# Kernel tuning notes

Hardware: AMD Instinct MI355X
Metric: run time of the kernel (lower is better)

The kernel has to match this reference:

```python
import jax, jax.numpy as jnp
import numpy as np

EPS = 1e-7
N_NODES = 100000

# --- Lorentz model (c = 1), working at the origin o = (1, 0, ..., 0) ---

def expmap0(v_spatial):
    """Exp map at origin: tangent spatial part [N, d] -> hyperboloid point [N, d+1]."""
    nrm = jnp.sqrt(jnp.maximum(jnp.sum(v_spatial * v_spatial, axis=-1, keepdims=True), EPS))
    x0 = jnp.cosh(nrm)
    xs = jnp.sinh(nrm) / nrm * v_spatial
    return jnp.concatenate([x0, xs], axis=-1)


def logmap0(x):
    """Log map at origin: point [N, d+1] -> tangent spatial part [N, d]."""
    x0 = jnp.maximum(x[..., :1], 1.0 + EPS)
    xs = x[..., 1:]
    nrm = jnp.sqrt(jnp.maximum(jnp.sum(xs * xs, axis=-1, keepdims=True), EPS))
    return jnp.arccosh(x0) / nrm * xs


def sigmoid_nonlin(x):
    # log map -> sigmoid in tangent space -> exp map (c_in = c_out = 1)
    return expmap0(jax.nn.sigmoid(logmap0(x)))


def hgcn_layer(x, edge_index, W, b):
    """HGCN conv: tangent-space linear + mean aggregation over edges + exp map."""
    t = logmap0(x)                      # [N, d_in]
    h = t @ W + b                       # [N, d_out]
    src, dst = edge_index[0], edge_index[1]
    msg = h[src]                        # [E, d_out] gather
    agg = jax.ops.segment_sum(msg, dst, num_segments=N_NODES)
    deg = jax.ops.segment_sum(jnp.ones((edge_index.shape[1],), h.dtype), dst,
                              num_segments=N_NODES)
    agg = agg / jnp.maximum(deg, 1.0)[:, None]
    return expmap0(agg)


def setup_inputs() -> dict:
    key = jax.random.key(0)
    ks = jax.random.split(key, 10)
    d_in, h1, h2, h_mlp, d_out = 64, 64, 64, 128, 40
    return {
        "features": jax.random.normal(ks[0], (N_NODES, d_in), jnp.float32),
        "edge_index": jax.random.randint(ks[1], (2, 1600000), 0, N_NODES, jnp.int64),
        "W1": jax.random.normal(ks[2], (d_in, h1), jnp.float32) * 0.05,
        "b1": jnp.zeros((h1,), jnp.float32),
        "W2": jax.random.normal(ks[3], (h1, h2), jnp.float32) * 0.05,
        "b2": jnp.zeros((h2,), jnp.float32),
        "W3": jax.random.normal(ks[4], (h2, h_mlp), jnp.float32) * 0.05,
        "b3": jnp.zeros((h_mlp,), jnp.float32),
        "W4": jax.random.normal(ks[5], (h_mlp, d_out), jnp.float32) * 0.05,
        "b4": jnp.zeros((d_out,), jnp.float32),
    }


def reference(features, edge_index, W1, b1, W2, b2, W3, b3, W4, b4):
    # lift Euclidean features to the hyperboloid (pad time coord, exp map)
    x = expmap0(features)                       # [N, d_in+1]
    x = hgcn_layer(x, edge_index, W1, b1)
    x = sigmoid_nonlin(x)
    x = hgcn_layer(x, edge_index, W2, b2)
    x = sigmoid_nonlin(x)
    t = logmap0(x)                              # [N, h2] (spatial part, drops time coord)
    # MLP head (dropout inactive at eval)
    h = jax.nn.relu(t @ W3 + b3)
    return h @ W4 + b4
```

## Files before the change

kernel.cpp:

```cpp
#include <hip/hip_runtime.h>


constexpr int CSHIFT = 9;
constexpr int CNODES = 1 << CSHIFT;
constexpr int EPB    = 4096;
constexpr int EPT    = EPB / 256;
constexpr int CAP    = 16384;

constexpr int W1F_OFF = 0;
constexpr int W2F_OFF = 4096;
constexpr int W3F_OFF = 8192;
constexpr int W4F_OFF = 16384;
constexpr int WIMG_TOT = 22528;

typedef __attribute__((ext_vector_type(8))) short short8;
typedef __attribute__((ext_vector_type(4))) float floatx4;

__device__ __forceinline__ float sigmoidf(float x) {
    return 1.0f / (1.0f + __expf(-x));
}
__device__ __forceinline__ unsigned short f2bf(float f) {
    unsigned int u = __float_as_uint(f);
    u = (u + 0x7FFFu + ((u >> 16) & 1u)) >> 16;
    return (unsigned short)u;
}

__global__ __launch_bounds__(256) void part_prep_k(
    const int* __restrict__ src, const int* __restrict__ dst,
    int* __restrict__ ccur, int* __restrict__ arena, int E, int NBUCK, int gP,
    const float* __restrict__ feat, unsigned short* __restrict__ featbf,
    const float* __restrict__ W1, const float* __restrict__ W2,
    const float* __restrict__ W3, const float* __restrict__ W4,
    unsigned short* __restrict__ img, int n8)
{
    __shared__ int  hist[256];
    __shared__ int  exoff[256];
    __shared__ int  lcur[256];
    __shared__ int  gbase[256];
    __shared__ int  stage[EPB];
    __shared__ unsigned char stageB[EPB];

    const int tid = threadIdx.x;

    if ((int)blockIdx.x >= gP) {
        int i = ((int)blockIdx.x - gP) * 256 + tid;
        if (i < n8) {
            const float4* p = (const float4*)feat + (size_t)i * 2;
            float4 a = p[0], b = p[1];
            uint4 o;
            o.x = (unsigned)f2bf(a.x) | ((unsigned)f2bf(a.y) << 16);
            o.y = (unsigned)f2bf(a.z) | ((unsigned)f2bf(a.w) << 16);
            o.z = (unsigned)f2bf(b.x) | ((unsigned)f2bf(b.y) << 16);
            o.w = (unsigned)f2bf(b.z) | ((unsigned)f2bf(b.w) << 16);
            ((uint4*)featbf)[i] = o;
            return;
        }
        int t = i - n8;
        if (t >= WIMG_TOT) return;
        float v = 0.f;
        int s = t;
        if (s < W2F_OFF) {
            int j = s & 7, m = (s >> 3) & 15, q = (s >> 7) & 3, kk = (s >> 9) & 1, c = s >> 10;
            v = W1[(kk * 32 + q * 8 + j) * 64 + c * 16 + m];
        } else if (s < W3F_OFF) {
            s -= W2F_OFF;
            int j = s & 7, m = (s >> 3) & 15, q = (s >> 7) & 3, kk = (s >> 9) & 1, c = s >> 10;
            v = W2[(kk * 32 + q * 8 + j) * 64 + c * 16 + m];
        } else if (s < W4F_OFF) {
            s -= W3F_OFF;
            int j = s & 7, m = (s >> 3) & 15, q = (s >> 7) & 3, kk = (s >> 9) & 1, c = s >> 10;
            v = W3[(kk * 32 + q * 8 + j) * 128 + c * 16 + m];
        } else {
            s -= W4F_OFF;
            int j = s & 7, m = (s >> 3) & 15, q = (s >> 7) & 3, kk = (s >> 9) & 3, c = s >> 11;
            int n = c * 16 + m;
            if (n < 40) v = W4[(kk * 32 + q * 8 + j) * 40 + n];
        }
        img[t] = f2bf(v);
        return;
    }

    const int e0  = blockIdx.x * EPB;
    const int ec  = min(EPB, E - e0);

    int pk[EPT], bk[EPT];
    hist[tid] = 0;
    __syncthreads();
    #pragma unroll
    for (int j = 0; j < EPT; j++) {
        int idx = tid + j * 256;
        if (idx < ec) {
            int s = src[e0 + idx];
            int d = dst[e0 + idx];
            bk[j] = d >> CSHIFT;
            pk[j] = s | ((d & (CNODES - 1)) << 17);
            atomicAdd(&hist[bk[j]], 1);
        } else bk[j] = -1;
    }
    __syncthreads();
    const int h = hist[tid];
    exoff[tid] = h;
    __syncthreads();
    for (int dd = 1; dd < 256; dd <<= 1) {
        int v = 0;
        if (tid >= dd) v = exoff[tid - dd];
        __syncthreads();
        if (tid >= dd) exoff[tid] += v;
        __syncthreads();
    }
    const int ex = exoff[tid] - h;
    int gb = 0;
    if (tid < NBUCK && h > 0) gb = atomicAdd(ccur + tid, h);
    __syncthreads();
    exoff[tid] = ex;
    lcur[tid]  = ex;
    gbase[tid] = gb;
    __syncthreads();
    #pragma unroll
    for (int j = 0; j < EPT; j++) {
        if (bk[j] >= 0) {
            int l = atomicAdd(&lcur[bk[j]], 1);
            stage[l]  = pk[j];
            stageB[l] = (unsigned char)bk[j];
        }
    }
    __syncthreads();
    for (int i = tid; i < ec; i += 256) {
        int b = stageB[i];
        arena[(size_t)b * CAP + gbase[b] + (i - exoff[b])] = stage[i];
    }
}

__global__ __launch_bounds__(1024) void csr_fine(const int* __restrict__ arena,
                                                 const int* __restrict__ ccur,
                                                 int* __restrict__ off,
                                                 int* __restrict__ ssrc,
                                                 int N, int E, int NBUCK) {
    __shared__ int part[256];
    __shared__ int cnt[CNODES];
    __shared__ int cur[CNODES];
    __shared__ int wpre[8];
    const int b = blockIdx.x;
    const int node0 = b << CSHIFT;
    const int tid = threadIdx.x;
    const int lane = tid & 63, wid = tid >> 6;

    if (tid < 256) part[tid] = (tid < NBUCK) ? ccur[tid] : 0;
    __syncthreads();
    for (int d = 1; d < 256; d <<= 1) {
        int v = 0;
        if (tid < 256 && tid >= d) v = part[tid - d];
        __syncthreads();
        if (tid < 256 && tid >= d) part[tid] += v;
        __syncthreads();
    }
    const int cbeg = (b > 0) ? part[b - 1] : 0;
    const int ec   = min(ccur[b], CAP);
    if (b == 0 && tid == 0) off[N] = E;

    if (tid < CNODES) cnt[tid] = 0;
    __syncthreads();
    const int* pe = arena + (size_t)b * CAP;
    for (int i = tid; i < ec; i += 1024)
        atomicAdd(&cnt[(pe[i] >> 17) & (CNODES - 1)], 1);
    __syncthreads();

    int c = (tid < CNODES) ? cnt[tid] : 0;
    int v = c;
    #pragma unroll
    for (int d = 1; d < 64; d <<= 1) {
        int t = __shfl_up(v, d);
        if (lane >= d) v += t;
    }
    if (tid < CNODES && lane == 63) wpre[wid] = v;
    __syncthreads();
    if (tid == 0) {
        int s = 0;
        #pragma unroll
        for (int k = 0; k < CNODES / 64; k++) { int t = wpre[k]; wpre[k] = s; s += t; }
    }
    __syncthreads();
    if (tid < CNODES) {
        int ex = wpre[wid] + v - c;
        cur[tid] = ex;
        int node = node0 + tid;
        if (node < N) off[node] = cbeg + ex;
    }
    __syncthreads();
    for (int i = tid; i < ec; i += 1024) {
        int p = pe[i];
        int pos = cbeg + atomicAdd(&cur[(p >> 17) & (CNODES - 1)], 1);
        ssrc[pos] = p & 0x1FFFF;
    }
}

#define ACC8(v)                                    \
    acc[0] += __uint_as_float((v).x << 16);        \
    acc[1] += __uint_as_float((v).x & 0xFFFF0000u);\
    acc[2] += __uint_as_float((v).y << 16);        \
    acc[3] += __uint_as_float((v).y & 0xFFFF0000u);\
    acc[4] += __uint_as_float((v).z << 16);        \
    acc[5] += __uint_as_float((v).z & 0xFFFF0000u);\
    acc[6] += __uint_as_float((v).w << 16);        \
    acc[7] += __uint_as_float((v).w & 0xFFFF0000u);

__device__ __forceinline__ void gather_tile_wave(
    const unsigned short* __restrict__ h, const int* __restrict__ off,
    const int* __restrict__ ssrc, unsigned short* Agg, int rowB, int N,
    int w, int lane)
{
    #pragma unroll
    for (int pass = 0; pass < 2; pass++) {
        int rl = w * 16 + pass * 8 + (lane >> 3);
        int g  = rowB + rl;
        int q  = (lane & 7) * 8;
        uint4 p = make_uint4(0u, 0u, 0u, 0u);
        if (g < N) {
            int beg = off[g], end = off[g + 1];
            float acc[8] = {0.f, 0.f, 0.f, 0.f, 0.f, 0.f, 0.f, 0.f};
            int i = beg;
            for (; i + 8 <= end; i += 8) {
                uint4 v0 = *(const uint4*)(h + (size_t)ssrc[i]     * 64 + q);
                uint4 v1 = *(const uint4*)(h + (size_t)ssrc[i + 1] * 64 + q);
                uint4 v2 = *(const uint4*)(h + (size_t)ssrc[i + 2] * 64 + q);
                uint4 v3 = *(const uint4*)(h + (size_t)ssrc[i + 3] * 64 + q);
                uint4 v4 = *(const uint4*)(h + (size_t)ssrc[i + 4] * 64 + q);
                uint4 v5 = *(const uint4*)(h + (size_t)ssrc[i + 5] * 64 + q);
                uint4 v6 = *(const uint4*)(h + (size_t)ssrc[i + 6] * 64 + q);
                uint4 v7 = *(const uint4*)(h + (size_t)ssrc[i + 7] * 64 + q);
                ACC8(v0); ACC8(v1); ACC8(v2); ACC8(v3);
                ACC8(v4); ACC8(v5); ACC8(v6); ACC8(v7);
            }
            for (; i + 2 <= end; i += 2) {
                uint4 v0 = *(const uint4*)(h + (size_t)ssrc[i]     * 64 + q);
                uint4 v1 = *(const uint4*)(h + (size_t)ssrc[i + 1] * 64 + q);
                ACC8(v0); ACC8(v1);
            }
            for (; i < end; i++) {
                uint4 v = *(const uint4*)(h + (size_t)ssrc[i] * 64 + q);
                ACC8(v);
            }
            float inv = __builtin_amdgcn_rcpf((float)max(end - beg, 1));
            p.x = (unsigned)f2bf(acc[0]*inv) | ((unsigned)f2bf(acc[1]*inv) << 16);
            p.y = (unsigned)f2bf(acc[2]*inv) | ((unsigned)f2bf(acc[3]*inv) << 16);
            p.z = (unsigned)f2bf(acc[4]*inv) | ((unsigned)f2bf(acc[5]*inv) << 16);
            p.w = (unsigned)f2bf(acc[6]*inv) | ((unsigned)f2bf(acc[7]*inv) << 16);
        }
        *(uint4*)(Agg + rl * 72 + q) = p;
    }
}

__global__ __launch_bounds__(128) void aggemm1_k(
    const unsigned short* __restrict__ featbf, const int* __restrict__ off,
    const int* __restrict__ ssrc, const unsigned short* __restrict__ img,
    const float* __restrict__ bias, unsigned short* __restrict__ t1, int N)
{
    __shared__ alignas(16) unsigned short Agg[32 * 72];

    const int tid = threadIdx.x;
    const int rowB = blockIdx.x * 32;
    const int w = tid >> 6, lane = tid & 63;
    const int m = lane & 15, quad = lane >> 4;
    const int row0 = rowB + w * 16;

    gather_tile_wave(featbf, off, ssrc, Agg, rowB, N, w, lane);

    const short8* Wf = (const short8*)(img + W1F_OFF);
    floatx4 acc[4];
    #pragma unroll
    for (int c = 0; c < 4; c++) acc[c] = (floatx4){0.f, 0.f, 0.f, 0.f};
    #pragma unroll
    for (int kk = 0; kk < 2; kk++) {
        short8 a = *(const short8*)(Agg + (w * 16 + m) * 72 + kk * 32 + quad * 8);
        #pragma unroll
        for (int c = 0; c < 4; c++) {
            short8 b = Wf[((c * 2 + kk) * 4 + quad) * 16 + m];
            acc[c] = __builtin_amdgcn_mfma_f32_16x16x32_bf16(a, b, acc[c], 0, 0, 0);
        }
    }
    bool dzr[4];
    int rows[4];
    #pragma unroll
    for (int r = 0; r < 4; r++) {
        rows[r] = row0 + quad * 4 + r;
        dzr[r] = (rows[r] < N) ? (off[rows[r] + 1] == off[rows[r]]) : false;
    }
    #pragma unroll
    for (int c = 0; c < 4; c++) {
        int col = c * 16 + m;
        float bv = bias[col];
        #pragma unroll
        for (int r = 0; r < 4; r++) {
            if (rows[r] < N) {
                float v = dzr[r] ? 0.5f : sigmoidf(acc[c][r] + bv);
                t1[(size_t)rows[r] * 64 + col] = f2bf(v);
            }
        }
    }
}

__global__ __launch_bounds__(128) void aggep3_k(
    const unsigned short* __restrict__ t1, const int* __restrict__ off,
    const int* __restrict__ ssrc, const unsigned short* __restrict__ img,
    const float* __restrict__ b2, const float* __restrict__ b3,
    const float* __restrict__ b4, float* __restrict__ out, int N)
{
    __shared__ alignas(16) unsigned short SM[4608];
    unsigned short* T2  = SM;
    unsigned short* Agg = SM + 2304;
    unsigned short* H3h = SM + 2304;

    const int tid = threadIdx.x;
    const int rowB = blockIdx.x * 32;
    const int w = tid >> 6, lane = tid & 63;
    const int m = lane & 15, quad = lane >> 4;
    const int row0 = rowB + w * 16;

    gather_tile_wave(t1, off, ssrc, Agg, rowB, N, w, lane);

    {
        const short8* Wf = (const short8*)(img + W2F_OFF);
        floatx4 acc[4];
        #pragma unroll
        for (int c = 0; c < 4; c++) acc[c] = (floatx4){0.f, 0.f, 0.f, 0.f};
        #pragma unroll
        for (int kk = 0; kk < 2; kk++) {
            short8 a = *(const short8*)(Agg + (w * 16 + m) * 72 + kk * 32 + quad * 8);
            #pragma unroll
            for (int c = 0; c < 4; c++) {
                short8 b = Wf[((c * 2 + kk) * 4 + quad) * 16 + m];
                acc[c] = __builtin_amdgcn_mfma_f32_16x16x32_bf16(a, b, acc[c], 0, 0, 0);
            }
        }
        bool dzr[4];
        #pragma unroll
        for (int r = 0; r < 4; r++) {
            int row = row0 + quad * 4 + r;
            dzr[r] = (row < N) ? (off[row + 1] == off[row]) : false;
        }
        #pragma unroll
        for (int c = 0; c < 4; c++) {
            int col = c * 16 + m;
            float bv = b2[col];
            #pragma unroll
            for (int r = 0; r < 4; r++) {
                int rl = w * 16 + quad * 4 + r;
                float v = dzr[r] ? 0.5f : sigmoidf(acc[c][r] + bv);
                T2[rl * 72 + col] = f2bf(v);
            }
        }
    }

    floatx4 acc2[3];
    #pragma unroll
    for (int c = 0; c < 3; c++) acc2[c] = (floatx4){0.f, 0.f, 0.f, 0.f};
    const short8* Wf3 = (const short8*)(img + W3F_OFF);
    const short8* Wf4 = (const short8*)(img + W4F_OFF);

    #pragma unroll
    for (int half = 0; half < 2; half++) {
        floatx4 acc[4];
        #pragma unroll
        for (int c = 0; c < 4; c++) acc[c] = (floatx4){0.f, 0.f, 0.f, 0.f};
        #pragma unroll
        for (int kk = 0; kk < 2; kk++) {
            short8 a = *(const short8*)(T2 + (w * 16 + m) * 72 + kk * 32 + quad * 8);
            #pragma unroll
            for (int c = 0; c < 4; c++) {
                short8 b = Wf3[(((half * 4 + c) * 2 + kk) * 4 + quad) * 16 + m];
                acc[c] = __builtin_amdgcn_mfma_f32_16x16x32_bf16(a, b, acc[c], 0, 0, 0);
            }
        }
        #pragma unroll
        for (int c = 0; c < 4; c++) {
            int col = c * 16 + m;
            float bv = b3[half * 64 + col];
            #pragma unroll
            for (int r = 0; r < 4; r++) {
                int rl = w * 16 + quad * 4 + r;
                H3h[rl * 72 + col] = f2bf(fmaxf(acc[c][r] + bv, 0.f));
            }
        }
        #pragma unroll
        for (int kk2 = 0; kk2 < 2; kk2++) {
            short8 a = *(const short8*)(H3h + (w * 16 + m) * 72 + kk2 * 32 + quad * 8);
            #pragma unroll
            for (int c = 0; c < 3; c++) {
                short8 b = Wf4[((c * 4 + half * 2 + kk2) * 4 + quad) * 16 + m];
                acc2[c] = __builtin_amdgcn_mfma_f32_16x16x32_bf16(a, b, acc2[c], 0, 0, 0);
            }
        }
    }

    #pragma unroll
    for (int c = 0; c < 3; c++) {
        int col = c * 16 + m;
        if (col < 40) {
            float bv = b4[col];
            #pragma unroll
            for (int r = 0; r < 4; r++) {
                int row = row0 + quad * 4 + r;
                if (row < N) out[(size_t)row * 40 + col] = acc2[c][r] + bv;
            }
        }
    }
}

extern "C" void kernel_launch(void* const* d_in, const int* in_sizes, int n_in,
                              void* d_out, int out_size, void* d_ws, size_t ws_size,
                              hipStream_t stream)
{
    const float* feat = (const float*)d_in[0];
    const int*   eidx = (const int*)d_in[1];
    const float* W1 = (const float*)d_in[2];
    const float* b1 = (const float*)d_in[3];
    const float* W2 = (const float*)d_in[4];
    const float* b2 = (const float*)d_in[5];
    const float* W3 = (const float*)d_in[6];
    const float* b3 = (const float*)d_in[7];
    const float* W4 = (const float*)d_in[8];
    const float* b4 = (const float*)d_in[9];

    const int N = in_sizes[0] / 64;
    const int E = in_sizes[1] / 2;
    const int* src = eidx;
    const int* dst = eidx + E;

    const int NBUCK = (N + CNODES - 1) / CNODES;

    unsigned short* featbf = (unsigned short*)d_ws;
    unsigned short* t1     = featbf + (size_t)N * 64;
    unsigned short* img    = t1     + (size_t)N * 64;
    int*   off   = (int*)(img + WIMG_TOT);
    int*   ccur  = off + (N + 1);
    int*   ssrc  = ccur + NBUCK;
    int*   arena = ssrc + E;
    float* out   = (float*)d_out;

    hipMemsetAsync(ccur, 0, (size_t)NBUCK * sizeof(int), stream);

    const dim3 blk(256);
    const int gP  = (E + EPB - 1) / EPB;
    const int g32 = (N + 31) / 32;
    const int n8  = N * 64 / 8;
    const int gPC = (n8 + WIMG_TOT + 255) / 256;

    part_prep_k<<<gP + gPC, blk, 0, stream>>>(src, dst, ccur, arena, E, NBUCK,
                                              gP, feat, featbf, W1, W2, W3, W4,
                                              img, n8);
    csr_fine<<<NBUCK, dim3(1024), 0, stream>>>(arena, ccur, off, ssrc, N, E, NBUCK);

    aggemm1_k<<<g32, dim3(128), 0, stream>>>(featbf, off, ssrc, img, b1, t1, N);
    aggep3_k<<<g32, dim3(128), 0, stream>>>(t1, off, ssrc, img, b2, b3, b4, out, N);
}
```

Measured before the change: 219.1 us.

## Widen partition kernel, use wave-shuffle scan, deepen gather unroll

Raises the partition/prep kernel to 512 threads per block, so each thread handles fewer edges and the conversion blocks cover more elements. It also replaces the shared-memory Hillis-Steele bucket scan, which synchronised on every step, with a wave-level shuffle scan plus a tiny per-wave prefix. Separately, the neighbour gather loop now loads 16 source indices first and then issues 16 row loads, with a 4-wide remainder loop, to put more memory requests in flight. The costs are higher register pressure in the gather and fewer concurrent partition blocks per CU.

```diff
diff --git a/kernel.cpp b/kernel.cpp
--- a/kernel.cpp
+++ b/kernel.cpp
@@ -4,7 +4,8 @@
 constexpr int CSHIFT = 9;
 constexpr int CNODES = 1 << CSHIFT;
 constexpr int EPB    = 4096;
-constexpr int EPT    = EPB / 256;
+constexpr int PTHR   = 512;
+constexpr int EPT    = EPB / PTHR;
 constexpr int CAP    = 16384;
 
 constexpr int W1F_OFF = 0;
@@ -25,7 +26,7 @@
     return (unsigned short)u;
 }
 
-__global__ __launch_bounds__(256) void part_prep_k(
+__global__ __launch_bounds__(512) void part_prep_k(
     const int* __restrict__ src, const int* __restrict__ dst,
     int* __restrict__ ccur, int* __restrict__ arena, int E, int NBUCK, int gP,
     const float* __restrict__ feat, unsigned short* __restrict__ featbf,
@@ -37,13 +38,14 @@
     __shared__ int  exoff[256];
     __shared__ int  lcur[256];
     __shared__ int  gbase[256];
+    __shared__ int  wsum[4];
     __shared__ int  stage[EPB];
     __shared__ unsigned char stageB[EPB];
 
     const int tid = threadIdx.x;
 
     if ((int)blockIdx.x >= gP) {
-        int i = ((int)blockIdx.x - gP) * 256 + tid;
+        int i = ((int)blockIdx.x - gP) * PTHR + tid;
         if (i < n8) {
             const float4* p = (const float4*)feat + (size_t)i * 2;
             float4 a = p[0], b = p[1];
@@ -82,13 +84,14 @@
 
     const int e0  = blockIdx.x * EPB;
     const int ec  = min(EPB, E - e0);
+    const int lane = tid & 63, wid = tid >> 6;
 
     int pk[EPT], bk[EPT];
-    hist[tid] = 0;
+    if (tid < 256) hist[tid] = 0;
     __syncthreads();
     #pragma unroll
     for (int j = 0; j < EPT; j++) {
-        int idx = tid + j * 256;
+        int idx = tid + j * PTHR;
         if (idx < ec) {
             int s = src[e0 + idx];
             int d = dst[e0 + idx];
@@ -98,23 +101,32 @@
         } else bk[j] = -1;
     }
     __syncthreads();
-    const int h = hist[tid];
-    exoff[tid] = h;
-    __syncthreads();
-    for (int dd = 1; dd < 256; dd <<= 1) {
-        int v = 0;
-        if (tid >= dd) v = exoff[tid - dd];
-        __syncthreads();
-        if (tid >= dd) exoff[tid] += v;
-        __syncthreads();
-    }
-    const int ex = exoff[tid] - h;
-    int gb = 0;
-    if (tid < NBUCK && h > 0) gb = atomicAdd(ccur + tid, h);
-    __syncthreads();
-    exoff[tid] = ex;
-    lcur[tid]  = ex;
-    gbase[tid] = gb;
+    int h = 0, v = 0;
+    if (tid < 256) {
+        h = hist[tid];
+        v = h;
+        #pragma unroll
+        for (int d = 1; d < 64; d <<= 1) {
+            int t = __shfl_up(v, d);
+            if (lane >= d) v += t;
+        }
+        if (lane == 63) wsum[wid] = v;
+    }
+    __syncthreads();
+    if (tid == 0) {
+        int s = 0;
+        #pragma unroll
+        for (int k = 0; k < 4; k++) { int t = wsum[k]; wsum[k] = s; s += t; }
+    }
+    __syncthreads();
+    if (tid < 256) {
+        int ex = wsum[wid] + v - h;
+        int gb = 0;
+        if (tid < NBUCK && h > 0) gb = atomicAdd(ccur + tid, h);
+        exoff[tid] = ex;
+        lcur[tid]  = ex;
+        gbase[tid] = gb;
+    }
     __syncthreads();
     #pragma unroll
     for (int j = 0; j < EPT; j++) {
@@ -125,7 +137,7 @@
         }
     }
     __syncthreads();
-    for (int i = tid; i < ec; i += 256) {
+    for (int i = tid; i < ec; i += PTHR) {
         int b = stageB[i];
         arena[(size_t)b * CAP + gbase[b] + (i - exoff[b])] = stage[i];
     }
@@ -219,22 +231,44 @@
             int beg = off[g], end = off[g + 1];
             float acc[8] = {0.f, 0.f, 0.f, 0.f, 0.f, 0.f, 0.f, 0.f};
             int i = beg;
-            for (; i + 8 <= end; i += 8) {
-                uint4 v0 = *(const uint4*)(h + (size_t)ssrc[i]     * 64 + q);
-                uint4 v1 = *(const uint4*)(h + (size_t)ssrc[i + 1] * 64 + q);
-                uint4 v2 = *(const uint4*)(h + (size_t)ssrc[i + 2] * 64 + q);
-                uint4 v3 = *(const uint4*)(h + (size_t)ssrc[i + 3] * 64 + q);
-                uint4 v4 = *(const uint4*)(h + (size_t)ssrc[i + 4] * 64 + q);
-                uint4 v5 = *(const uint4*)(h + (size_t)ssrc[i + 5] * 64 + q);
-                uint4 v6 = *(const uint4*)(h + (size_t)ssrc[i + 6] * 64 + q);
-                uint4 v7 = *(const uint4*)(h + (size_t)ssrc[i + 7] * 64 + q);
+            for (; i + 16 <= end; i += 16) {
+                int s0 = ssrc[i],      s1 = ssrc[i + 1];
+                int s2 = ssrc[i + 2],  s3 = ssrc[i + 3];
+                int s4 = ssrc[i + 4],  s5 = ssrc[i + 5];
+                int s6 = ssrc[i + 6],  s7 = ssrc[i + 7];
+                int s8 = ssrc[i + 8],  s9 = ssrc[i + 9];
+                int sa = ssrc[i + 10], sb = ssrc[i + 11];
+                int sc = ssrc[i + 12], sd = ssrc[i + 13];
+                int se = ssrc[i + 14], sf = ssrc[i + 15];
+                uint4 v0 = *(const uint4*)(h + (size_t)s0 * 64 + q);
+                uint4 v1 = *(const uint4*)(h + (size_t)s1 * 64 + q);
+                uint4 v2 = *(const uint4*)(h + (size_t)s2 * 64 + q);
+                uint4 v3 = *(const uint4*)(h + (size_t)s3 * 64 + q);
+                uint4 v4 = *(const uint4*)(h + (size_t)s4 * 64 + q);
+                uint4 v5 = *(const uint4*)(h + (size_t)s5 * 64 + q);
+                uint4 v6 = *(const uint4*)(h + (size_t)s6 * 64 + q);
+                uint4 v7 = *(const uint4*)(h + (size_t)s7 * 64 + q);
+                uint4 v8 = *(const uint4*)(h + (size_t)s8 * 64 + q);
+                uint4 v9 = *(const uint4*)(h + (size_t)s9 * 64 + q);
+                uint4 va = *(const uint4*)(h + (size_t)sa * 64 + q);
+                uint4 vb = *(const uint4*)(h + (size_t)sb * 64 + q);
+                uint4 vc = *(const uint4*)(h + (size_t)sc * 64 + q);
+                uint4 vd = *(const uint4*)(h + (size_t)sd * 64 + q);
+                uint4 ve = *(const uint4*)(h + (size_t)se * 64 + q);
+                uint4 vf = *(const uint4*)(h + (size_t)sf * 64 + q);
                 ACC8(v0); ACC8(v1); ACC8(v2); ACC8(v3);
                 ACC8(v4); ACC8(v5); ACC8(v6); ACC8(v7);
-            }
-            for (; i + 2 <= end; i += 2) {
-                uint4 v0 = *(const uint4*)(h + (size_t)ssrc[i]     * 64 + q);
-                uint4 v1 = *(const uint4*)(h + (size_t)ssrc[i + 1] * 64 + q);
-                ACC8(v0); ACC8(v1);
+                ACC8(v8); ACC8(v9); ACC8(va); ACC8(vb);
+                ACC8(vc); ACC8(vd); ACC8(ve); ACC8(vf);
+            }
+            for (; i + 4 <= end; i += 4) {
+                int s0 = ssrc[i],     s1 = ssrc[i + 1];
+                int s2 = ssrc[i + 2], s3 = ssrc[i + 3];
+                uint4 v0 = *(const uint4*)(h + (size_t)s0 * 64 + q);
+                uint4 v1 = *(const uint4*)(h + (size_t)s1 * 64 + q);
+                uint4 v2 = *(const uint4*)(h + (size_t)s2 * 64 + q);
+                uint4 v3 = *(const uint4*)(h + (size_t)s3 * 64 + q);
+                ACC8(v0); ACC8(v1); ACC8(v2); ACC8(v3);
             }
             for (; i < end; i++) {
                 uint4 v = *(const uint4*)(h + (size_t)ssrc[i] * 64 + q);
@@ -439,15 +473,14 @@
 
     hipMemsetAsync(ccur, 0, (size_t)NBUCK * sizeof(int), stream);
 
-    const dim3 blk(256);
     const int gP  = (E + EPB - 1) / EPB;
     const int g32 = (N + 31) / 32;
     const int n8  = N * 64 / 8;
-    const int gPC = (n8 + WIMG_TOT + 255) / 256;
-
-    part_prep_k<<<gP + gPC, blk, 0, stream>>>(src, dst, ccur, arena, E, NBUCK,
-                                              gP, feat, featbf, W1, W2, W3, W4,
-                                              img, n8);
+    const int gPC = (n8 + WIMG_TOT + PTHR - 1) / PTHR;
+
+    part_prep_k<<<gP + gPC, dim3(PTHR), 0, stream>>>(src, dst, ccur, arena, E,
+                                                     NBUCK, gP, feat, featbf,
+                                                     W1, W2, W3, W4, img, n8);
     csr_fine<<<NBUCK, dim3(1024), 0, stream>>>(arena, ccur, off, ssrc, N, E, NBUCK);
 
     aggemm1_k<<<g32, dim3(128), 0, stream>>>(featbf, off, ssrc, img, b1, t1, N);
```

Result: slower. 225.6 us (+3.0%).
